# Kernel tuning notes

Hardware: AMD Instinct MI355X
Metric: run time of the kernel (lower is better)

## Reference

```python
import jax, jax.numpy as jnp
import numpy as np
from jax import lax

IMG = 224.0
IOU_THRESH = 0.5

def box_cxcywh_to_xyxy(b):
    cx, cy, w, h = b[..., 0], b[..., 1], b[..., 2], b[..., 3]
    return jnp.stack([cx - 0.5 * w, cy - 0.5 * h, cx + 0.5 * w, cy + 0.5 * h], axis=-1)

def box_iou(a, b):
    area_a = (a[:, 2] - a[:, 0]) * (a[:, 3] - a[:, 1])
    area_b = (b[:, 2] - b[:, 0]) * (b[:, 3] - b[:, 1])
    lt = jnp.maximum(a[:, None, :2], b[None, :, :2])
    rb = jnp.minimum(a[:, None, 2:], b[None, :, 2:])
    wh = jnp.clip(rb - lt, 0.0)
    inter = wh[..., 0] * wh[..., 1]
    return inter / (area_a[:, None] + area_b[None, :] - inter)

def gumbel_softmax(key, logits, axis, tau=1.0):
    # straight-through hard gumbel-softmax (matches torch hard=True)
    g = jax.random.gumbel(key, logits.shape, logits.dtype)
    y = jax.nn.softmax((logits + g) / tau, axis=axis)
    y_hard = jax.nn.one_hot(jnp.argmax(y, axis=axis), y.shape[axis], axis=axis, dtype=y.dtype)
    return y + lax.stop_gradient(y_hard - y)

def nms_indices(boxes, scores, thresh):
    # iterative greedy NMS, returns kept indices in descending-score order (as torchvision)
    n = boxes.shape[0]
    order = jnp.argsort(-scores)
    b = boxes[order]
    areas = (b[:, 2] - b[:, 0]) * (b[:, 3] - b[:, 1])
    pos = jnp.arange(n)
    def body(i, suppressed):
        bi = b[i]
        lt = jnp.maximum(bi[:2], b[:, :2])
        rb = jnp.minimum(bi[2:], b[:, 2:])
        wh = jnp.clip(rb - lt, 0.0)
        inter = wh[:, 0] * wh[:, 1]
        iou = inter / (areas[i] + areas - inter)
        sup = (iou > thresh) & (pos > i) & jnp.logical_not(suppressed[i])
        return suppressed | sup
    suppressed = lax.fori_loop(0, n, body, jnp.zeros((n,), bool))
    keep = np.asarray(jnp.logical_not(suppressed))
    return jnp.asarray(np.asarray(order)[keep])

def _keys():
    return jax.random.split(jax.random.key(42), 3)

def _boxes_and_scores(classencodings, pred_logits, pred_boxes, tgt_ids, batch_idx, tgt_bbox, k0):
    C = classencodings.shape[0]
    B, Q, D = pred_logits.shape
    similarity = jnp.einsum('bqd,cd->bqc', pred_logits, classencodings)
    out_scores = jnp.max(similarity, axis=-1)
    clt = gumbel_softmax(k0, similarity, axis=-1)                      # [B,Q,C] hard
    offx = jnp.arange(C, dtype=pred_logits.dtype) * IMG
    offy = jnp.arange(B, dtype=pred_logits.dtype) * IMG
    ox = jnp.sum(clt * offx, axis=-1)                                  # [B,Q]
    oy = jnp.broadcast_to(offy[:, None], (B, Q))
    out_off = jnp.tile(jnp.stack([ox, oy], axis=-1), (1, 1, 2))        # [B,Q,4]
    out_bbox = (box_cxcywh_to_xyxy(pred_boxes) + out_off).reshape(-1, 4)
    f = pred_logits.dtype
    gt_off = jnp.tile(jnp.stack([IMG * tgt_ids.astype(f), IMG * batch_idx.astype(f)], axis=-1), (1, 2))
    tb = box_cxcywh_to_xyxy(tgt_bbox) + gt_off                         # [N,4]
    return similarity, out_scores.reshape(-1), out_bbox, tb

def ce_diag(logits):
    # CrossEntropyLoss(mean) with targets arange(n)
    return -jnp.mean(jnp.diagonal(jax.nn.log_softmax(logits, axis=1)))

def _forward(classencodings, pred_logits, pred_boxes, pred_masks, tgt_masks, tgt_embs, tgt_bbox, tgt_ids, batch_idx, nms_idx):
    k0, k1, k2 = _keys()
    B, Q, D = pred_logits.shape
    N = tgt_embs.shape[0]
    W, H = tgt_masks.shape[-2:]
    similarity, out_scores, out_bbox, tb = _boxes_and_scores(classencodings, pred_logits, pred_boxes, tgt_ids, batch_idx, tgt_bbox, k0)
    kept = out_bbox[nms_idx]                                           # [K,4]
    K = kept.shape[0]
    iou = box_iou(kept, tb)
    iou = jnp.where(jnp.isnan(iou), 0.0, iou)
    gt_log = jax.nn.softmax(iou, axis=1)
    gt_one_hot = gumbel_softmax(k1, gt_log, axis=1)                    # [K,N]
    gt_sel = gt_one_hot.T @ kept                                       # [N,4]
    gt_ious = jnp.diagonal(box_iou(gt_sel, tb))
    out_embs = gt_one_hot.T @ pred_logits.reshape(-1, D)[nms_idx]      # [N,D]
    class_loss = ce_diag(tgt_embs @ out_embs.T) + ce_diag(out_embs @ tgt_embs.T)
    scores = jnp.einsum('bqd,nd->bqn', pred_logits, tgt_embs).reshape(B * Q, N)
    ind = gumbel_softmax(k2, scores, axis=0).T                         # [N,B*Q]
    om = (ind @ pred_masks.reshape(B * Q, -1)).reshape(N, W, H)
    overall_mask_loss = jnp.mean((om - tgt_masks) ** 2)
    ocm = jnp.einsum('qwh,bcq->bcwh', om, similarity) / om.shape[1]    # [B,Q,W,H] (N==C==Q)
    ocm = jax.nn.softmax(ocm, axis=1)
    batch_lookup = jax.nn.one_hot(batch_idx, B, dtype=pred_logits.dtype).T  # [B,N]
    gt_sim = tgt_embs @ classencodings.T                               # [N,C]
    tsim = batch_lookup[:, :, None] * gt_sim[None, :, :]               # [B,N,C]
    gt_cm = jnp.einsum('bnc,nwh->bcwh', tsim, tgt_masks)               # [B,C,W,H]
    inp = ocm.reshape(B, -1)
    tgt = gt_cm.reshape(B, -1)
    dice = jnp.mean(jnp.sum(inp * tgt) / (jnp.sum(inp, -1) + jnp.sum(tgt, -1) + 1e-6))
    l1 = jnp.abs(gt_sel - tb).sum()
    return jnp.stack([class_loss, dice, overall_mask_loss / K, (1.0 - gt_ious).sum() / K, l1 / K])

def setup_inputs():
    key = jax.random.key(0)
    ks = jax.random.split(key, 10)
    B, Q, C, N, D, W, H = 8, 300, 300, 300, 256, 96, 96
    return {
        'classencodings': jax.random.normal(ks[0], (C, D), jnp.float32),
        'pred_logits': jax.random.normal(ks[1], (B, Q, D), jnp.float32),
        'pred_boxes': jax.random.uniform(ks[2], (B, Q, 4), jnp.float32),
        'pred_masks': jax.random.normal(ks[3], (B * Q, W, H), jnp.float32),
        'tgt_masks': jax.random.uniform(ks[4], (N, W, H), jnp.float32),
        'tgt_embs': jax.random.normal(ks[5], (N, D), jnp.float32),
        'tgt_bbox': jax.random.uniform(ks[6], (N, 4), jnp.float32),
        'im_masks': jnp.ones((B, 224, 224), jnp.float32),
        'tgt_ids': jax.random.randint(ks[7], (N,), 0, C, jnp.int32),
        'batch_idx': jnp.sort(jax.random.randint(ks[8], (N,), 0, B, jnp.int32)),
    }

def reference(classencodings, pred_logits, pred_boxes, pred_masks, tgt_masks, tgt_embs, tgt_bbox, im_masks, tgt_ids, batch_idx):
    k0, _, _ = _keys()
    _, scores, out_bbox, _ = _boxes_and_scores(classencodings, pred_logits, pred_boxes, tgt_ids, batch_idx, tgt_bbox, k0)
    nms_idx = nms_indices(out_bbox, scores, IOU_THRESH)
    return _forward(classencodings, pred_logits, pred_boxes, pred_masks, tgt_masks, tgt_embs, tgt_bbox, tgt_ids, batch_idx, nms_idx)
```

## Files before the change

kernel.cpp:

```cpp
#include <hip/hip_runtime.h>
#include <stdint.h>

#define DEVFN __device__ __forceinline__

typedef unsigned short u16;
typedef short bf16x8 __attribute__((ext_vector_type(8)));
typedef float f32x4 __attribute__((ext_vector_type(4)));

constexpr int BB = 8, QQ = 300, CC = 300, NN = 300, DD = 256;
constexpr int WHX = 9216, BQ = 2400, SIMW = 600;
constexpr int QP = 320;
constexpr int CP = 304;
constexpr int KP = 96;
constexpr int NP = 416;
constexpr int CELLCAP = 300;

constexpr size_t F_SIMS   = 0;
constexpr size_t F_GTSIM  = F_SIMS   + (size_t)BQ*SIMW;
constexpr size_t F_MM     = F_GTSIM  + (size_t)NN*CC;
constexpr size_t F_SCORE  = F_MM     + (size_t)NN*NN;
constexpr size_t F_BBOX   = F_SCORE  + BQ;
constexpr size_t F_TB     = F_BBOX   + (size_t)BQ*4;
constexpr size_t F_SB     = F_TB     + (size_t)NN*4;
constexpr size_t F_SAREA  = F_SB     + (size_t)BQ*4;
constexpr size_t F_KB     = F_SAREA  + BQ;
constexpr size_t F_ROWSUM = F_KB     + (size_t)BQ*4;
constexpr size_t F_OE     = F_ROWSUM + NN;
constexpr size_t F_GSEL   = F_OE     + (size_t)NN*DD;
constexpr size_t F_MSUM   = F_GSEL   + (size_t)NN*4;
constexpr size_t F_STGT   = F_MSUM   + NN;
constexpr size_t F_SC     = F_STGT   + 8;
constexpr size_t F_CNT    = F_SC     + 16;
constexpr size_t F_ACCEND = F_CNT    + BQ;
constexpr size_t F_ORDER  = F_ACCEND;
constexpr size_t F_NMSIDX = F_ORDER  + BQ;
constexpr size_t F_SEL2   = F_NMSIDX + BQ;
constexpr size_t F_BSTART = F_SEL2   + NN;
constexpr size_t F_KINT   = F_BSTART + 16;
constexpr size_t F_CLS    = F_KINT   + 4;
constexpr size_t F_KEEPF  = F_CLS    + BQ;
constexpr size_t F_LIST   = F_KEEPF  + BQ;
constexpr size_t F_S2T    = F_LIST   + (size_t)BQ*CELLCAP;
constexpr size_t F_SIMTB  = ((F_S2T + (size_t)NN*BQ + 7) & ~(size_t)7);
constexpr size_t F_OMT    = F_SIMTB + (size_t)BB*CP*QP/2;
constexpr size_t F_TMT    = F_OMT   + (size_t)WHX*QP/2;
constexpr size_t F_GTP    = F_TMT   + (size_t)WHX*NP/2;
constexpr size_t F_TOTAL  = F_GTP   + (size_t)BB*CP*KP/2;

DEVFN uint32_t rotl32(uint32_t v, int r){ return (v << r) | (v >> (32 - r)); }

DEVFN void tf2x32(uint32_t k0, uint32_t k1, uint32_t x0, uint32_t x1,
                  uint32_t& o0, uint32_t& o1){
  uint32_t ks2 = k0 ^ k1 ^ 0x1BD11BDAu;
  x0 += k0; x1 += k1;
#define TFR(r) x0 += x1; x1 = rotl32(x1, r); x1 ^= x0;
  TFR(13) TFR(15) TFR(26) TFR(6)   x0 += k1;  x1 += ks2 + 1u;
  TFR(17) TFR(29) TFR(16) TFR(24)  x0 += ks2; x1 += k0  + 2u;
  TFR(13) TFR(15) TFR(26) TFR(6)   x0 += k0;  x1 += k1  + 3u;
  TFR(17) TFR(29) TFR(16) TFR(24)  x0 += k1;  x1 += ks2 + 4u;
  TFR(13) TFR(15) TFR(26) TFR(6)   x0 += ks2; x1 += k0  + 5u;
#undef TFR
  o0 = x0; o1 = x1;
}

DEVFN void subkey(int i, uint32_t& k0, uint32_t& k1){
  tf2x32(0u, 42u, 0u, (uint32_t)i, k0, k1);
}

DEVFN float gumbel32(uint32_t k0, uint32_t k1, uint32_t idx){
  uint32_t h, l; tf2x32(k0, k1, 0u, idx, h, l);
  uint32_t bits = h ^ l;
  float f = __uint_as_float((bits >> 9) | 0x3F800000u) - 1.0f;
  const float tiny = 1.17549435e-38f;
  float u = fmaxf(tiny, f + tiny);
  return -logf(-logf(u));
}

DEVFN float iou_xyxy(float ax1,float ay1,float ax2,float ay2,
                     float bx1,float by1,float bx2,float by2){
  float aa = (ax2-ax1)*(ay2-ay1);
  float ab = (bx2-bx1)*(by2-by1);
  float lx = fmaxf(ax1,bx1), ly = fmaxf(ay1,by1);
  float rx = fminf(ax2,bx2), ry = fminf(ay2,by2);
  float iw = fmaxf(rx-lx,0.f), ih = fmaxf(ry-ly,0.f);
  float in_ = iw*ih;
  return in_/(aa+ab-in_);
}

DEVFN u16 f2bf(float x){
  uint32_t u = __float_as_uint(x);
  uint32_t r = u + 0x7FFFu + ((u >> 16) & 1u);
  return (u16)(r >> 16);
}

DEVFN void gload_lds16(const u16* g, u16* l){
  __builtin_amdgcn_global_load_lds(
      (const __attribute__((address_space(1))) unsigned int*)g,
      (__attribute__((address_space(3))) unsigned int*)l,
      16, 0, 0);
}

__global__ __launch_bounds__(256) void k_gemm_t(
    const float* __restrict__ pl, const float* __restrict__ ce,
    const float* __restrict__ te, float* __restrict__ sims,
    float* __restrict__ gtsim, float* __restrict__ s2t){
  __shared__ float As[16][64];
  __shared__ float Bs[16][64];
  const int row0 = blockIdx.x * 64, col0 = blockIdx.y * 64;
  const int tid = threadIdx.x;
  const int lrow = tid >> 2, lk0 = (tid & 3) * 4;
  const int tr = tid >> 4, tc = tid & 15;

  float acc[4][4];
  #pragma unroll
  for (int i = 0; i < 4; i++)
    #pragma unroll
    for (int j = 0; j < 4; j++) acc[i][j] = 0.f;

  const float4 z4 = {0.f,0.f,0.f,0.f};
  const int grow = row0 + lrow;
  const int gcol = col0 + lrow;
  const float* arow = nullptr;
  if (grow < 2400) arow = pl + (size_t)grow * DD;
  else if (grow < 2700) arow = te + (size_t)(grow - 2400) * DD;
  const float* brow = nullptr;
  if (gcol < 300) brow = ce + (size_t)gcol * DD;
  else if (gcol < 600) brow = te + (size_t)(gcol - 300) * DD;

  float4 av = arow ? *(const float4*)(arow + lk0) : z4;
  float4 bv = brow ? *(const float4*)(brow + lk0) : z4;

  for (int step = 0; step < 16; step++){
    __syncthreads();
    #pragma unroll
    for (int j = 0; j < 4; j++){
      As[lk0 + j][lrow] = ((const float*)&av)[j];
      Bs[lk0 + j][lrow] = ((const float*)&bv)[j];
    }
    __syncthreads();
    if (step + 1 < 16){
      const int k0 = (step + 1) * 16;
      av = arow ? *(const float4*)(arow + k0 + lk0) : z4;
      bv = brow ? *(const float4*)(brow + k0 + lk0) : z4;
    }
    #pragma unroll
    for (int kk = 0; kk < 16; kk++){
      float4 a4 = *(const float4*)&As[kk][tr*4];
      float4 b4 = *(const float4*)&Bs[kk][tc*4];
      float a[4] = {a4.x,a4.y,a4.z,a4.w};
      float b[4] = {b4.x,b4.y,b4.z,b4.w};
      #pragma unroll
      for (int i = 0; i < 4; i++)
        #pragma unroll
        for (int j = 0; j < 4; j++)
          acc[i][j] = fmaf(a[i], b[j], acc[i][j]);
    }
  }

  #pragma unroll
  for (int i = 0; i < 4; i++){
    const int r = row0 + tr*4 + i;
    const int c0 = col0 + tc*4;
    if (r < 2400){
      if (c0 < 600){
        float4 o0 = {acc[i][0],acc[i][1],acc[i][2],acc[i][3]};
        *(float4*)(sims + (size_t)r*SIMW + c0) = o0;
        if (c0 >= 300){
          #pragma unroll
          for (int j = 0; j < 4; j++)
            s2t[(size_t)(c0 + j - 300)*BQ + r] = acc[i][j];
        }
      }
    } else if (r < 2700){
      const int n = r - 2400;
      #pragma unroll
      for (int j = 0; j < 4; j++){
        int c = c0 + j;
        if (c < 300) gtsim[(size_t)n*CC + c] = acc[i][j];
      }
    }
  }
}

__global__ __launch_bounds__(256) void k_post(
    const float* __restrict__ sims, const float* __restrict__ pb,
    const float* __restrict__ tbb, const int* __restrict__ tids,
    const int* __restrict__ bidx, const float* __restrict__ gtsim,
    float* __restrict__ score, float* __restrict__ bbox,
    float* __restrict__ tb, float* __restrict__ rowsum,
    int* __restrict__ clsout){
  int bq = blockIdx.x, tid = threadIdx.x;
  __shared__ float sv[256];
  __shared__ int   si[256];
  const int i2 = tid + 256;
  float v1 = (tid < CC) ? sims[(size_t)bq*SIMW + tid] : -INFINITY;
  float v2 = (i2  < CC) ? sims[(size_t)bq*SIMW + i2]  : -INFINITY;
  sv[tid] = fmaxf(v1, v2); __syncthreads();
  for (int s = 128; s > 0; s >>= 1){ if (tid < s) sv[tid] = fmaxf(sv[tid], sv[tid+s]); __syncthreads(); }
  if (tid == 0) score[bq] = sv[0];
  __syncthreads();
  uint32_t gk0, gk1; subkey(0, gk0, gk1);
  float y1 = (tid < CC) ? v1 + gumbel32(gk0, gk1, (uint32_t)(bq*CC + tid)) : -INFINITY;
  float y2 = (i2  < CC) ? v2 + gumbel32(gk0, gk1, (uint32_t)(bq*CC + i2))  : -INFINITY;
  float ym; int yi;
  if (y2 > y1){ ym = y2; yi = i2; } else { ym = y1; yi = tid; }
  sv[tid] = ym; si[tid] = yi; __syncthreads();
  for (int s = 128; s > 0; s >>= 1){
    if (tid < s){
      float ov = sv[tid+s]; int oi = si[tid+s];
      if (ov > sv[tid] || (ov == sv[tid] && oi < si[tid])){ sv[tid] = ov; si[tid] = oi; }
    }
    __syncthreads();
  }
  if (tid == 0){
    int cls = si[0];
    clsout[bq] = cls;
    float ox = 224.0f * (float)cls;
    float oy = 224.0f * (float)(bq / QQ);
    float cx = pb[bq*4+0], cy = pb[bq*4+1], ww = pb[bq*4+2], hh = pb[bq*4+3];
    bbox[bq*4+0] = cx - 0.5f*ww + ox;
    bbox[bq*4+1] = cy - 0.5f*hh + oy;
    bbox[bq*4+2] = cx + 0.5f*ww + ox;
    bbox[bq*4+3] = cy + 0.5f*hh + oy;
  }
  if (bq < NN){
    __syncthreads();
    float r1 = (tid < CC) ? gtsim[(size_t)bq*CC + tid] : 0.f;
    float r2 = (i2  < CC) ? gtsim[(size_t)bq*CC + i2]  : 0.f;
    sv[tid] = r1 + r2; __syncthreads();
    for (int s = 128; s > 0; s >>= 1){ if (tid < s) sv[tid] += sv[tid+s]; __syncthreads(); }
    if (tid == 0) rowsum[bq] = sv[0];
    if (tid == 1){
      float gx = 224.0f * (float)tids[bq], gy = 224.0f * (float)bidx[bq];
      float cx = tbb[bq*4+0], cy = tbb[bq*4+1], ww = tbb[bq*4+2], hh = tbb[bq*4+3];
      tb[bq*4+0] = cx - 0.5f*ww + gx;
      tb[bq*4+1] = cy - 0.5f*hh + gy;
      tb[bq*4+2] = cx + 0.5f*ww + gx;
      tb[bq*4+3] = cy + 0.5f*hh + gy;
    }
  }
}

__global__ __launch_bounds__(256) void k_rankgather(
    const float* __restrict__ score, const float* __restrict__ bbox,
    const int* __restrict__ cls, const int* __restrict__ bidx,
    int* __restrict__ order, float* __restrict__ sb,
    int* __restrict__ bstart, int* __restrict__ cnt,
    int* __restrict__ list){
  const int t = blockIdx.x;
  const int tid = threadIdx.x;
  const float st = score[t];
  int c = 0;
  for (int j = tid; j < BQ; j += 256){
    float sj = score[j];
    c += (sj > st) || (sj == st && j < t);
  }
  __shared__ int red[256];
  red[tid] = c; __syncthreads();
  for (int s = 128; s > 0; s >>= 1){
    if (tid < s) red[tid] += red[tid+s];
    __syncthreads();
  }
  if (tid == 0){
    int r = red[0];
    order[r] = t;
    float x1 = bbox[t*4+0], y1 = bbox[t*4+1], x2 = bbox[t*4+2], y2 = bbox[t*4+3];
    sb[r*4+0] = x1; sb[r*4+1] = y1; sb[r*4+2] = x2; sb[r*4+3] = y2;
    int key = (t / QQ) * CC + cls[t];
    int slot = atomicAdd(&cnt[key], 1);
    list[(size_t)key*CELLCAP + slot] = r;
  }
  if (t == 0 && tid >= 32 && tid < 41){
    int b = tid - 32, cb = 0;
    for (int n = 0; n < NN; n++) cb += (bidx[n] < b);
    bstart[b] = cb;
  }
}

__global__ __launch_bounds__(256) void k_cellnms(
    const float* __restrict__ sb, const int* __restrict__ cnt,
    const int* __restrict__ list, int* __restrict__ keepf){
  int key = blockIdx.x*256 + threadIdx.x;
  if (key >= BB*CC) return;
  int m = cnt[key];
  if (m <= 0) return;
  const int* lst = list + (size_t)key*CELLCAP;
  unsigned long long keptmask = 0ull;
  int prevp = -1;
  for (int a = 0; a < m; a++){
    int pa = 0x7fffffff;
    for (int j = 0; j < m; j++){
      int pj = lst[j];
      if (pj > prevp && pj < pa) pa = pj;
    }
    prevp = pa;
    float4 A = ((const float4*)sb)[pa];
    float areaA = (A.z-A.x)*(A.w-A.y);
    bool kept = true;
    int pbprev = -1;
    for (int b2 = 0; b2 < a; b2++){
      int pb = 0x7fffffff;
      for (int j = 0; j < m; j++){
        int pj = lst[j];
        if (pj > pbprev && pj < pb) pb = pj;
      }
      pbprev = pb;
      bool keptb = (m <= 64) ? (((keptmask >> b2) & 1ull) != 0ull) : (keepf[pb] != 0);
      if (!keptb) continue;
      float4 B = ((const float4*)sb)[pb];
      float areaB = (B.z-B.x)*(B.w-B.y);
      float lx = fmaxf(A.x,B.x), ly = fmaxf(A.y,B.y);
      float rx = fminf(A.z,B.z), ry = fminf(A.w,B.w);
      float iw = fmaxf(rx-lx,0.f), ih = fmaxf(ry-ly,0.f);
      float inter = iw*ih;
      if (inter/(areaA + areaB - inter) > 0.5f){ kept = false; break; }
    }
    if (m <= 64 && kept) keptmask |= (1ull << a);
    keepf[pa] = kept ? 1 : 0;
  }
}

__global__ __launch_bounds__(256) void k_compact(
    const int* __restrict__ keepflag, const int* __restrict__ order,
    const float* __restrict__ sb, int* __restrict__ nmsidx,
    float* __restrict__ kb, int* __restrict__ kint){
  __shared__ int csum[256];
  int tid = threadIdx.x;
  int p0 = tid*10;
  int keepf[10];
  int cnt = 0;
  #pragma unroll
  for (int d = 0; d < 10; d++){
    int p = p0 + d;
    int k = 0;
    if (p < BQ) k = keepflag[p];
    keepf[d] = k; cnt += k;
  }
  csum[tid] = cnt; __syncthreads();
  for (int s = 1; s < 256; s <<= 1){
    int add = (tid >= s) ? csum[tid - s] : 0;
    __syncthreads();
    csum[tid] += add;
    __syncthreads();
  }
  int pos = csum[tid] - cnt;
  #pragma unroll
  for (int d = 0; d < 10; d++){
    if (keepf[d]){
      int p = p0 + d;
      nmsidx[pos] = order[p];
      ((float4*)kb)[pos] = ((const float4*)sb)[p];
      pos++;
    }
  }
  if (tid == 255) kint[0] = csum[255];
}

__global__ __launch_bounds__(512) void k_gtsel(
    const float* __restrict__ kb, const float* __restrict__ tb,
    const int* __restrict__ nmsidx, const float* __restrict__ pl,
    const int* __restrict__ kint, float* __restrict__ gsel,
    float* __restrict__ oe){
  int k = blockIdx.x;
  if (k >= kint[0]) return;
  int tid = threadIdx.x;
  __shared__ float sv[512];
  __shared__ int   si[512];
  float4 a = ((const float4*)kb)[k];
  float iou = -INFINITY;
  if (tid < NN){
    float4 t = ((const float4*)tb)[tid];
    iou = iou_xyxy(a.x,a.y,a.z,a.w, t.x,t.y,t.z,t.w);
    if (iou != iou) iou = 0.f;
  }
  sv[tid] = iou; __syncthreads();
  for (int s = 256; s > 0; s >>= 1){ if (tid < s) sv[tid] = fmaxf(sv[tid], sv[tid+s]); __syncthreads(); }
  float m = sv[0]; __syncthreads();
  float e = (tid < NN) ? expf(iou - m) : 0.f;
  sv[tid] = e; __syncthreads();
  for (int s = 256; s > 0; s >>= 1){ if (tid < s) sv[tid] += sv[tid+s]; __syncthreads(); }
  float S = sv[0]; __syncthreads();
  uint32_t gk0, gk1; subkey(1, gk0, gk1);
  float y = (tid < NN) ? (e / S + gumbel32(gk0, gk1, (uint32_t)(k*NN + tid))) : -INFINITY;
  sv[tid] = y; si[tid] = tid; __syncthreads();
  for (int s = 256; s > 0; s >>= 1){
    if (tid < s){
      float ov = sv[tid+s]; int oi = si[tid+s];
      if (ov > sv[tid] || (ov == sv[tid] && oi < si[tid])){ sv[tid] = ov; si[tid] = oi; }
    }
    __syncthreads();
  }
  int sel = si[0];
  if (tid < 4) atomicAdd(&gsel[sel*4 + tid], ((const float*)&a)[tid]);
  if (tid < DD) atomicAdd(&oe[(size_t)sel*DD + tid], pl[(size_t)nmsidx[k]*DD + tid]);
}

__global__ __launch_bounds__(256) void k_m_t(
    const float* __restrict__ te, const float* __restrict__ oe,
    float* __restrict__ M){
  __shared__ float As[16][32];
  __shared__ float Bs[16][32];
  const int row0 = blockIdx.x * 32, col0 = blockIdx.y * 32;
  const int tid = threadIdx.x;
  const int lr = tid >> 3, lk0 = (tid & 7) * 2;
  const int tr = tid >> 4, tc = tid & 15;
  float acc[2][2] = {{0.f,0.f},{0.f,0.f}};
  const float* arow = (row0 + lr < NN) ? te + (size_t)(row0 + lr)*DD : nullptr;
  const float* brow = (col0 + lr < NN) ? oe + (size_t)(col0 + lr)*DD : nullptr;
  for (int step = 0; step < 16; step++){
    const int k0 = step*16;
    float2 a2 = arow ? *(const float2*)(arow + k0 + lk0) : float2{0.f,0.f};
    float2 b2 = brow ? *(const float2*)(brow + k0 + lk0) : float2{0.f,0.f};
    __syncthreads();
    As[lk0][lr] = a2.x; As[lk0+1][lr] = a2.y;
    Bs[lk0][lr] = b2.x; Bs[lk0+1][lr] = b2.y;
    __syncthreads();
    #pragma unroll
    for (int kk = 0; kk < 16; kk++){
      float a0 = As[kk][tr*2], a1 = As[kk][tr*2+1];
      float b0 = Bs[kk][tc*2], b1 = Bs[kk][tc*2+1];
      acc[0][0] = fmaf(a0,b0,acc[0][0]);
      acc[0][1] = fmaf(a0,b1,acc[0][1]);
      acc[1][0] = fmaf(a1,b0,acc[1][0]);
      acc[1][1] = fmaf(a1,b1,acc[1][1]);
    }
  }
  #pragma unroll
  for (int i = 0; i < 2; i++){
    int r = row0 + tr*2 + i;
    if (r >= NN) continue;
    #pragma unroll
    for (int j = 0; j < 2; j++){
      int c = col0 + tc*2 + j;
      if (c < NN) M[(size_t)r*NN + c] = acc[i][j];
    }
  }
}

__global__ __launch_bounds__(64) void k_ce(
    const float* __restrict__ M, float* __restrict__ sc){
  int i = blockIdx.x, lane = threadIdx.x;
  float m = -INFINITY;
  for (int j = lane; j < NN; j += 64) m = fmaxf(m, M[(size_t)i*NN + j]);
  for (int o = 32; o > 0; o >>= 1) m = fmaxf(m, __shfl_xor(m, o));
  float s = 0.f;
  for (int j = lane; j < NN; j += 64) s += expf(M[(size_t)i*NN + j] - m);
  for (int o = 32; o > 0; o >>= 1) s += __shfl_xor(s, o);
  float lr = m + logf(s);
  float m2 = -INFINITY;
  for (int j = lane; j < NN; j += 64) m2 = fmaxf(m2, M[(size_t)j*NN + i]);
  for (int o = 32; o > 0; o >>= 1) m2 = fmaxf(m2, __shfl_xor(m2, o));
  float s2 = 0.f;
  for (int j = lane; j < NN; j += 64) s2 += expf(M[(size_t)j*NN + i] - m2);
  for (int o = 32; o > 0; o >>= 1) s2 += __shfl_xor(s2, o);
  float lc = m2 + logf(s2);
  if (lane == 0){
    float d = M[(size_t)i*NN + i];
    atomicAdd(&sc[0], lr - d);
    atomicAdd(&sc[1], lc - d);
  }
}

__global__ __launch_bounds__(256) void k_sel2(
    const float* __restrict__ s2t, int* __restrict__ sel2){
  int n = blockIdx.x, tid = threadIdx.x;
  uint32_t gk0, gk1; subkey(2, gk0, gk1);
  float best = -INFINITY; int bi = 0x7fffffff;
  for (int r = tid; r < BQ; r += 256){
    float v = s2t[(size_t)n*BQ + r] + gumbel32(gk0, gk1, (uint32_t)(r*NN + n));
    if (v > best){ best = v; bi = r; }
  }
  __shared__ float sv[256];
  __shared__ int   si[256];
  sv[tid] = best; si[tid] = bi; __syncthreads();
  for (int s = 128; s > 0; s >>= 1){
    if (tid < s){
      float ov = sv[tid+s]; int oi = si[tid+s];
      if (ov > sv[tid] || (ov == sv[tid] && oi < si[tid])){ sv[tid] = ov; si[tid] = oi; }
    }
    __syncthreads();
  }
  if (tid == 0) sel2[n] = si[0];
}

constexpr int PB_SIMT = 400;
constexpr int PB_OMT  = 1440;
constexpr int PB_TMT  = 1872;
constexpr int PB_GTP  = 114;
constexpr int PB_OM   = 2700;
__global__ __launch_bounds__(256) void k_pack(
    const float* __restrict__ sims, const float* __restrict__ pm,
    const float* __restrict__ tm, const float* __restrict__ gtsim,
    const int* __restrict__ sel2, const int* __restrict__ bstart,
    u16* __restrict__ simTb, u16* __restrict__ omT,
    u16* __restrict__ tmT, u16* __restrict__ gtp,
    float* __restrict__ msum, float* __restrict__ sc){
  __shared__ float ld[32][65];
  const int blk = blockIdx.x;
  const int tid = threadIdx.x;

  if (blk < PB_SIMT){
    int bx = blk % 10, by = (blk / 10) % 5, b = blk / 50;
    int q0 = bx*32, c0 = by*64;
    for (int i = tid; i < 32*64; i += 256){
      int qi = i >> 6, ci = i & 63;
      int q = q0 + qi, c = c0 + ci;
      ld[qi][ci] = (q < QQ && c < CC) ? sims[((size_t)b*QQ + q)*SIMW + c] : 0.f;
    }
    __syncthreads();
    int cloc = tid >> 2, j0 = (tid & 3)*8;
    int c = c0 + cloc;
    if (c < CP){
      u16 tmp[8];
      #pragma unroll
      for (int j = 0; j < 8; j++) tmp[j] = f2bf(ld[j0+j][cloc]);
      *(uint4*)(simTb + ((size_t)b*CP + c)*QP + q0 + j0) = *(const uint4*)tmp;
    }
  } else if (blk < PB_SIMT + PB_OMT){
    int r = blk - PB_SIMT;
    int q0 = (r % 10)*32, wh0 = (r / 10)*64;
    for (int i = tid; i < 32*64; i += 256){
      int qi = i >> 6, wi = i & 63;
      int q = q0 + qi;
      ld[qi][wi] = (q < QQ) ? pm[(size_t)sel2[q]*WHX + wh0 + wi] * (1.0f/96.0f) : 0.f;
    }
    __syncthreads();
    int wloc = tid >> 2, j0 = (tid & 3)*8;
    u16 tmp[8];
    #pragma unroll
    for (int j = 0; j < 8; j++) tmp[j] = f2bf(ld[j0+j][wloc]);
    *(uint4*)(omT + (size_t)(wh0+wloc)*QP + q0 + j0) = *(const uint4*)tmp;
  } else if (blk < PB_SIMT + PB_OMT + PB_TMT){
    int r = blk - PB_SIMT - PB_OMT;
    int n0 = (r % 13)*32, wh0 = (r / 13)*64;
    for (int i = tid; i < 32*64; i += 256){
      int ni = i >> 6, wi = i & 63;
      int n = n0 + ni;
      ld[ni][wi] = (n < NN) ? tm[(size_t)n*WHX + wh0 + wi] : 0.f;
    }
    __syncthreads();
    int wloc = tid >> 2, j0 = (tid & 3)*8;
    u16 tmp[8];
    #pragma unroll
    for (int j = 0; j < 8; j++) tmp[j] = f2bf(ld[j0+j][wloc]);
    *(uint4*)(tmT + (size_t)(wh0+wloc)*NP + n0 + j0) = *(const uint4*)tmp;
  } else if (blk < PB_SIMT + PB_OMT + PB_TMT + PB_GTP){
    int g = (blk - PB_SIMT - PB_OMT - PB_TMT)*256 + tid;
    int b = g / (CP*(KP/8));
    int rem = g - b*(CP*(KP/8));
    int c = rem / (KP/8);
    int kg = rem % (KP/8);
    int n0 = bstart[b], n1 = bstart[b+1];
    int kst = n0 & ~7;
    u16 tmp[8];
    #pragma unroll
    for (int j = 0; j < 8; j++){
      int n = kst + kg*8 + j;
      float v = (n >= n0 && n < n1 && c < CC) ? gtsim[(size_t)n*CC + c] : 0.f;
      tmp[j] = f2bf(v);
    }
    *(uint4*)(gtp + ((size_t)b*CP + c)*KP + kg*8) = *(const uint4*)tmp;
  } else {
    int nb = blk - (PB_SIMT + PB_OMT + PB_TMT + PB_GTP);
    int n = nb / 9, ch = nb % 9;
    int c0 = ch*1024 + tid*4;
    const float4 o4 = *(const float4*)(pm + (size_t)sel2[n]*WHX + c0);
    const float4 t4 = *(const float4*)(tm + (size_t)n*WHX + c0);
    float dx = o4.x-t4.x, dy = o4.y-t4.y, dz = o4.z-t4.z, dw = o4.w-t4.w;
    float d2 = dx*dx + dy*dy + dz*dz + dw*dw;
    float ts = t4.x + t4.y + t4.z + t4.w;
    float* r1 = &ld[0][0];
    float* r2 = r1 + 256;
    r1[tid] = d2; r2[tid] = ts; __syncthreads();
    for (int s = 128; s > 0; s >>= 1){
      if (tid < s){ r1[tid] += r1[tid+s]; r2[tid] += r2[tid+s]; }
      __syncthreads();
    }
    if (tid == 0){ atomicAdd(&sc[2], r1[0]); atomicAdd(&msum[n], r2[0]); }
  }
}

constexpr int ALDS = 32;
__global__ __launch_bounds__(256) void k_zsoft(
    const u16* __restrict__ simTb, const u16* __restrict__ omT,
    const u16* __restrict__ gtp, const u16* __restrict__ tmT,
    const int* __restrict__ bstart, float* __restrict__ sc){
  const int bid = blockIdx.x;
  const int xcd = bid & 7;
  const int r9  = bid >> 3;
  const int tile = xcd * 18 + (r9 % 18);
  const int b    = r9 / 18;
  const int tid = threadIdx.x;
  const int w = tid >> 6, l = tid & 63;
  const int lrow = l & 15, lgrp = l >> 4;
  const int col = tile*64 + w*16 + lrow;

  __shared__ u16 As[2][CP*ALDS];
  __shared__ float red[256];

  const u16* Ab = simTb + (size_t)b*CP*QP;
  int srcoff[5];
  #pragma unroll
  for (int i = 0; i < 5; i++){
    int p = (w*5 + i)*64 + l;
    int row = p >> 2, cs = p & 3;
    int g = cs ^ ((row >> 1) & 3);
    srcoff[i] = row*QP + g*8;
  }
  const int nIss = (w == 3) ? 4 : 5;
  const int roff = (lgrp ^ ((lrow >> 1) & 3)) << 3;
  const u16* pB = omT + (size_t)col*QP + lgrp*8;

  #pragma unroll
  for (int i = 0; i < 5; i++){
    if (i < nIss) gload_lds16(Ab + srcoff[i], &As[0][(w*5+i)*512]);
  }
  bf16x8 bcur = *(const bf16x8*)(pB);

  f32x4 acc[19];
  #pragma unroll
  for (int t = 0; t < 19; t++) acc[t] = (f32x4){0.f,0.f,0.f,0.f};
  __syncthreads();

  for (int ks = 0; ks < 10; ks++){
    const int cur = ks & 1;
    bf16x8 bnext;
    if (ks + 1 < 10){
      const int ko = (ks + 1) * 32;
      #pragma unroll
      for (int i = 0; i < 5; i++){
        if (i < nIss) gload_lds16(Ab + srcoff[i] + ko, &As[cur ^ 1][(w*5+i)*512]);
      }
      bnext = *(const bf16x8*)(pB + ko);
    }
    __builtin_amdgcn_s_setprio(1);
    #pragma unroll
    for (int t = 0; t < 19; t++){
      bf16x8 af = *(const bf16x8*)&As[cur][t*16*ALDS + lrow*ALDS + roff];
      acc[t] = __builtin_amdgcn_mfma_f32_16x16x32_bf16(af, bcur, acc[t], 0, 0, 0);
    }
    __builtin_amdgcn_s_setprio(0);
    bcur = bnext;
    __syncthreads();
  }

  const int n0 = bstart[b];
  const int kst = n0 & ~7;
  const u16* tB = tmT + (size_t)col*NP + kst + lgrp*8;
  bf16x8 b2a = *(const bf16x8*)(tB);
  bf16x8 b2b = *(const bf16x8*)(tB + 32);
  bf16x8 b2c = *(const bf16x8*)(tB + 64);
  const u16* A2 = gtp + (size_t)b*CP*KP + (size_t)lrow*KP + lgrp*8;
  bf16x8 ca0 = *(const bf16x8*)(A2);
  bf16x8 ca1 = *(const bf16x8*)(A2 + 32);
  bf16x8 ca2 = *(const bf16x8*)(A2 + 64);
  bf16x8 da0 = *(const bf16x8*)(A2 + 16*KP);
  bf16x8 da1 = *(const bf16x8*)(A2 + 16*KP + 32);
  bf16x8 da2 = *(const bf16x8*)(A2 + 16*KP + 64);

  float lmax = -INFINITY;
  #pragma unroll
  for (int t = 0; t < 19; t++){
    if (t == 18 && lgrp == 3) continue;
    lmax = fmaxf(lmax, fmaxf(fmaxf(acc[t][0], acc[t][1]), fmaxf(acc[t][2], acc[t][3])));
  }
  lmax = fmaxf(lmax, __shfl_xor(lmax, 16));
  lmax = fmaxf(lmax, __shfl_xor(lmax, 32));
  float ls = 0.f;
  #pragma unroll
  for (int t = 0; t < 19; t++){
    if (t == 18 && lgrp == 3){
      acc[t] = (f32x4){0.f,0.f,0.f,0.f};
      continue;
    }
    float p0 = __expf(acc[t][0] - lmax);
    float p1 = __expf(acc[t][1] - lmax);
    float p2 = __expf(acc[t][2] - lmax);
    float p3 = __expf(acc[t][3] - lmax);
    acc[t][0] = p0; acc[t][1] = p1; acc[t][2] = p2; acc[t][3] = p3;
    ls += p0 + p1 + p2 + p3;
  }
  float S = ls;
  S += __shfl_xor(S, 16);
  S += __shfl_xor(S, 32);
  float inv = 1.f / S;

  float dl = 0.f;
  #pragma unroll
  for (int t = 0; t < 19; t++){
    f32x4 rr = (f32x4){0.f,0.f,0.f,0.f};
    rr = __builtin_amdgcn_mfma_f32_16x16x32_bf16(ca0, b2a, rr, 0, 0, 0);
    rr = __builtin_amdgcn_mfma_f32_16x16x32_bf16(ca1, b2b, rr, 0, 0, 0);
    rr = __builtin_amdgcn_mfma_f32_16x16x32_bf16(ca2, b2c, rr, 0, 0, 0);
    dl += acc[t][0]*rr[0] + acc[t][1]*rr[1] + acc[t][2]*rr[2] + acc[t][3]*rr[3];
    ca0 = da0; ca1 = da1; ca2 = da2;
    if (t + 2 < 19){
      const u16* ar = A2 + (size_t)(t + 2)*16*KP;
      da0 = *(const bf16x8*)(ar);
      da1 = *(const bf16x8*)(ar + 32);
      da2 = *(const bf16x8*)(ar + 64);
    }
  }
  dl *= inv;

  red[tid] = dl; __syncthreads();
  for (int s = 128; s > 0; s >>= 1){
    if (tid < s) red[tid] += red[tid+s];
    __syncthreads();
  }
  if (tid == 0) atomicAdd(&sc[5], red[0]);
}

__global__ __launch_bounds__(512) void k_final3(
    const float* __restrict__ gsel, const float* __restrict__ tb,
    const int* __restrict__ bidx, const float* __restrict__ rowsum,
    const float* __restrict__ msum, const float* __restrict__ sc,
    const int* __restrict__ kint, float* __restrict__ out){
  int tid = threadIdx.x;
  __shared__ float s1[512], s2[512];
  __shared__ float stgt[8];
  if (tid < 8) stgt[tid] = 0.f;
  __syncthreads();
  float a1 = 0.f, a2 = 0.f;
  if (tid < NN){
    float4 g = ((const float4*)gsel)[tid];
    float4 t = ((const float4*)tb)[tid];
    float iou = iou_xyxy(g.x,g.y,g.z,g.w, t.x,t.y,t.z,t.w);
    a1 = 1.f - iou;
    a2 = fabsf(g.x-t.x) + fabsf(g.y-t.y) + fabsf(g.z-t.z) + fabsf(g.w-t.w);
    atomicAdd(&stgt[bidx[tid]], rowsum[tid] * msum[tid]);
  }
  s1[tid] = a1; s2[tid] = a2; __syncthreads();
  for (int s = 256; s > 0; s >>= 1){
    if (tid < s){ s1[tid] += s1[tid+s]; s2[tid] += s2[tid+s]; }
    __syncthreads();
  }
  if (tid == 0){
    float K = (float)kint[0];
    float cls = sc[0]/300.f + sc[1]/300.f;
    float stot = sc[5];
    float dice = 0.f;
    for (int b = 0; b < 8; b++) dice += stot / (9216.0f + stgt[b] + 1e-6f);
    dice *= (1.0f/8.0f);
    out[0] = cls;
    out[1] = dice;
    out[2] = (sc[2] / 2764800.0f) / K;
    out[3] = s1[0] / K;
    out[4] = s2[0] / K;
  }
}

extern "C" void kernel_launch(void* const* d_in, const int* in_sizes, int n_in,
                              void* d_out, int out_size, void* d_ws, size_t ws_size,
                              hipStream_t stream) {
  const float* ce  = (const float*)d_in[0];
  const float* pl  = (const float*)d_in[1];
  const float* pb  = (const float*)d_in[2];
  const float* pm  = (const float*)d_in[3];
  const float* tm  = (const float*)d_in[4];
  const float* te  = (const float*)d_in[5];
  const float* tbb = (const float*)d_in[6];
  const int*  tids = (const int*)d_in[8];
  const int*  bidx = (const int*)d_in[9];
  float* out = (float*)d_out;
  float* w = (float*)d_ws;

  if (ws_size < F_TOTAL * sizeof(float)) return;

  float* SIMS   = w + F_SIMS;
  float* GTSIM  = w + F_GTSIM;
  float* MM     = w + F_MM;
  float* SCORE  = w + F_SCORE;
  float* BBOX   = w + F_BBOX;
  float* TBOX   = w + F_TB;
  float* SB     = w + F_SB;
  float* KB     = w + F_KB;
  float* ROWSUM = w + F_ROWSUM;
  float* OE     = w + F_OE;
  float* GSEL   = w + F_GSEL;
  float* MSUM   = w + F_MSUM;
  float* SC     = w + F_SC;
  float* S2T    = w + F_S2T;
  int*   CNT    = (int*)(w + F_CNT);
  int*   ORDER  = (int*)(w + F_ORDER);
  int*   NMSIDX = (int*)(w + F_NMSIDX);
  int*   SEL2   = (int*)(w + F_SEL2);
  int*   BSTART = (int*)(w + F_BSTART);
  int*   KINT   = (int*)(w + F_KINT);
  int*   CLS    = (int*)(w + F_CLS);
  int*   KEEPF  = (int*)(w + F_KEEPF);
  int*   LIST   = (int*)(w + F_LIST);
  u16* SIMTB = (u16*)(w + F_SIMTB);
  u16* OMT   = (u16*)(w + F_OMT);
  u16* TMT   = (u16*)(w + F_TMT);
  u16* GTP   = (u16*)(w + F_GTP);

  hipMemsetAsync(w + F_OE, 0, (F_ACCEND - F_OE) * sizeof(float), stream);

  k_gemm_t<<<dim3(43, 10), 256, 0, stream>>>(pl, ce, te, SIMS, GTSIM, S2T);
  k_post<<<BQ, 256, 0, stream>>>(SIMS, pb, tbb, tids, bidx, GTSIM, SCORE, BBOX, TBOX, ROWSUM, CLS);
  k_rankgather<<<BQ, 256, 0, stream>>>(SCORE, BBOX, CLS, bidx, ORDER, SB, BSTART, CNT, LIST);
  k_sel2<<<NN, 256, 0, stream>>>(S2T, SEL2);
  k_pack<<<PB_SIMT + PB_OMT + PB_TMT + PB_GTP + PB_OM, 256, 0, stream>>>(
      SIMS, pm, tm, GTSIM, SEL2, BSTART, SIMTB, OMT, TMT, GTP, MSUM, SC);
  k_cellnms<<<(BB*CC + 255)/256, 256, 0, stream>>>(SB, CNT, LIST, KEEPF);
  k_compact<<<1, 256, 0, stream>>>(KEEPF, ORDER, SB, NMSIDX, KB, KINT);
  k_gtsel<<<BQ, 512, 0, stream>>>(KB, TBOX, NMSIDX, pl, KINT, GSEL, OE);
  k_m_t<<<dim3(10, 10), 256, 0, stream>>>(te, OE, MM);
  k_ce<<<NN, 64, 0, stream>>>(MM, SC);
  k_zsoft<<<dim3((WHX/64) * BB), 256, 0, stream>>>(SIMTB, OMT, GTP, TMT, BSTART, SC);
  k_final3<<<1, 512, 0, stream>>>(GSEL, TBOX, bidx, ROWSUM, MSUM, SC, KINT, out);
}
```

Before: 268.0 us.

## Split zsoft warp tiles into 2x2 row/column halves with cross-warp softmax reduction

Re-tiles the k_zsoft MFMA work so each warp computes two 16-column groups over half of the C rows, instead of one column group over all 19 row tiles. Each A fragment read from LDS now feeds two MFMAs, which halves LDS A traffic per MFMA. The softmax max and sum are combined across warp pairs through shared memory. CP is padded to 320 so the rows split evenly into 10+10 tiles. This adds extra barriers and a padded row tile that has to be masked, and the second-stage MFMA work per column group is now split across warps.

Result: no change. 273.2 us (+1.9%).

```diff
diff --git a/kernel.cpp b/kernel.cpp
--- a/kernel.cpp
+++ b/kernel.cpp
@@ -10,7 +10,7 @@
 constexpr int BB = 8, QQ = 300, CC = 300, NN = 300, DD = 256;
 constexpr int WHX = 9216, BQ = 2400, SIMW = 600;
 constexpr int QP = 320;
-constexpr int CP = 304;
+constexpr int CP = 320;
 constexpr int KP = 96;
 constexpr int NP = 416;
 constexpr int CELLCAP = 300;
@@ -486,7 +486,7 @@
 constexpr int PB_SIMT = 400;
 constexpr int PB_OMT  = 1440;
 constexpr int PB_TMT  = 1872;
-constexpr int PB_GTP  = 114;
+constexpr int PB_GTP  = 120;
 constexpr int PB_OM   = 2700;
 __global__ __launch_bounds__(256) void k_pack(
     const float* __restrict__ sims, const float* __restrict__ pm,
@@ -593,7 +593,9 @@
   const int tid = threadIdx.x;
   const int w = tid >> 6, l = tid & 63;
   const int lrow = l & 15, lgrp = l >> 4;
-  const int col = tile*64 + w*16 + lrow;
+  const int cg = w >> 1, rh = w & 1;
+  const int col0 = tile*64 + cg*32 + lrow;
+  const int t0 = rh * 10;
 
   __shared__ u16 As[2][CP*ALDS];
   __shared__ float red[256];
@@ -607,101 +609,127 @@
     int g = cs ^ ((row >> 1) & 3);
     srcoff[i] = row*QP + g*8;
   }
-  const int nIss = (w == 3) ? 4 : 5;
   const int roff = (lgrp ^ ((lrow >> 1) & 3)) << 3;
-  const u16* pB = omT + (size_t)col*QP + lgrp*8;
-
-  #pragma unroll
-  for (int i = 0; i < 5; i++){
-    if (i < nIss) gload_lds16(Ab + srcoff[i], &As[0][(w*5+i)*512]);
-  }
-  bf16x8 bcur = *(const bf16x8*)(pB);
-
-  f32x4 acc[19];
-  #pragma unroll
-  for (int t = 0; t < 19; t++) acc[t] = (f32x4){0.f,0.f,0.f,0.f};
+  const u16* pB0 = omT + (size_t)col0*QP + lgrp*8;
+  const u16* pB1 = omT + (size_t)(col0+16)*QP + lgrp*8;
+
+  #pragma unroll
+  for (int i = 0; i < 5; i++) gload_lds16(Ab + srcoff[i], &As[0][(w*5+i)*512]);
+  bf16x8 bcur0 = *(const bf16x8*)pB0;
+  bf16x8 bcur1 = *(const bf16x8*)pB1;
+
+  f32x4 acc0[10], acc1[10];
+  #pragma unroll
+  for (int t = 0; t < 10; t++){
+    acc0[t] = (f32x4){0.f,0.f,0.f,0.f};
+    acc1[t] = (f32x4){0.f,0.f,0.f,0.f};
+  }
   __syncthreads();
 
   for (int ks = 0; ks < 10; ks++){
     const int cur = ks & 1;
-    bf16x8 bnext;
+    bf16x8 bnext0, bnext1;
     if (ks + 1 < 10){
       const int ko = (ks + 1) * 32;
       #pragma unroll
-      for (int i = 0; i < 5; i++){
-        if (i < nIss) gload_lds16(Ab + srcoff[i] + ko, &As[cur ^ 1][(w*5+i)*512]);
-      }
-      bnext = *(const bf16x8*)(pB + ko);
+      for (int i = 0; i < 5; i++) gload_lds16(Ab + srcoff[i] + ko, &As[cur ^ 1][(w*5+i)*512]);
+      bnext0 = *(const bf16x8*)(pB0 + ko);
+      bnext1 = *(const bf16x8*)(pB1 + ko);
     }
     __builtin_amdgcn_s_setprio(1);
     #pragma unroll
-    for (int t = 0; t < 19; t++){
-      bf16x8 af = *(const bf16x8*)&As[cur][t*16*ALDS + lrow*ALDS + roff];
-      acc[t] = __builtin_amdgcn_mfma_f32_16x16x32_bf16(af, bcur, acc[t], 0, 0, 0);
+    for (int t = 0; t < 10; t++){
+      bf16x8 af = *(const bf16x8*)&As[cur][(t0 + t)*16*ALDS + lrow*ALDS + roff];
+      acc0[t] = __builtin_amdgcn_mfma_f32_16x16x32_bf16(af, bcur0, acc0[t], 0, 0, 0);
+      acc1[t] = __builtin_amdgcn_mfma_f32_16x16x32_bf16(af, bcur1, acc1[t], 0, 0, 0);
     }
     __builtin_amdgcn_s_setprio(0);
-    bcur = bnext;
-    __syncthreads();
-  }
+    bcur0 = bnext0; bcur1 = bnext1;
+    __syncthreads();
+  }
+
+  float lmax0 = -INFINITY, lmax1 = -INFINITY;
+  #pragma unroll
+  for (int t = 0; t < 10; t++){
+    int g = t0 + t;
+    if (g == 19 || (g == 18 && lgrp == 3)) continue;
+    lmax0 = fmaxf(lmax0, fmaxf(fmaxf(acc0[t][0], acc0[t][1]), fmaxf(acc0[t][2], acc0[t][3])));
+    lmax1 = fmaxf(lmax1, fmaxf(fmaxf(acc1[t][0], acc1[t][1]), fmaxf(acc1[t][2], acc1[t][3])));
+  }
+  lmax0 = fmaxf(lmax0, __shfl_xor(lmax0, 16));
+  lmax0 = fmaxf(lmax0, __shfl_xor(lmax0, 32));
+  lmax1 = fmaxf(lmax1, __shfl_xor(lmax1, 16));
+  lmax1 = fmaxf(lmax1, __shfl_xor(lmax1, 32));
+  if (l < 16){ red[w*32 + l] = lmax0; red[w*32 + 16 + l] = lmax1; }
+  __syncthreads();
+  float m0 = fmaxf(lmax0, red[(w^1)*32 + lrow]);
+  float m1 = fmaxf(lmax1, red[(w^1)*32 + 16 + lrow]);
+  __syncthreads();
+
+  float ls0 = 0.f, ls1 = 0.f;
+  #pragma unroll
+  for (int t = 0; t < 10; t++){
+    int g = t0 + t;
+    if (g == 19 || (g == 18 && lgrp == 3)){
+      acc0[t] = (f32x4){0.f,0.f,0.f,0.f};
+      acc1[t] = (f32x4){0.f,0.f,0.f,0.f};
+      continue;
+    }
+    #pragma unroll
+    for (int q = 0; q < 4; q++){
+      float p0 = __expf(acc0[t][q] - m0);
+      float p1 = __expf(acc1[t][q] - m1);
+      acc0[t][q] = p0; acc1[t][q] = p1;
+      ls0 += p0; ls1 += p1;
+    }
+  }
+  ls0 += __shfl_xor(ls0, 16); ls0 += __shfl_xor(ls0, 32);
+  ls1 += __shfl_xor(ls1, 16); ls1 += __shfl_xor(ls1, 32);
+  if (l < 16){ red[w*32 + l] = ls0; red[w*32 + 16 + l] = ls1; }
+  __syncthreads();
+  float S0 = ls0 + red[(w^1)*32 + lrow];
+  float S1 = ls1 + red[(w^1)*32 + 16 + lrow];
+  __syncthreads();
+  float inv0 = 1.f / S0, inv1 = 1.f / S1;
 
   const int n0 = bstart[b];
   const int kst = n0 & ~7;
-  const u16* tB = tmT + (size_t)col*NP + kst + lgrp*8;
-  bf16x8 b2a = *(const bf16x8*)(tB);
-  bf16x8 b2b = *(const bf16x8*)(tB + 32);
-  bf16x8 b2c = *(const bf16x8*)(tB + 64);
   const u16* A2 = gtp + (size_t)b*CP*KP + (size_t)lrow*KP + lgrp*8;
-  bf16x8 ca0 = *(const bf16x8*)(A2);
-  bf16x8 ca1 = *(const bf16x8*)(A2 + 32);
-  bf16x8 ca2 = *(const bf16x8*)(A2 + 64);
-  bf16x8 da0 = *(const bf16x8*)(A2 + 16*KP);
-  bf16x8 da1 = *(const bf16x8*)(A2 + 16*KP + 32);
-  bf16x8 da2 = *(const bf16x8*)(A2 + 16*KP + 64);
-
-  float lmax = -INFINITY;
-  #pragma unroll
-  for (int t = 0; t < 19; t++){
-    if (t == 18 && lgrp == 3) continue;
-    lmax = fmaxf(lmax, fmaxf(fmaxf(acc[t][0], acc[t][1]), fmaxf(acc[t][2], acc[t][3])));
-  }
-  lmax = fmaxf(lmax, __shfl_xor(lmax, 16));
-  lmax = fmaxf(lmax, __shfl_xor(lmax, 32));
-  float ls = 0.f;
-  #pragma unroll
-  for (int t = 0; t < 19; t++){
-    if (t == 18 && lgrp == 3){
-      acc[t] = (f32x4){0.f,0.f,0.f,0.f};
-      continue;
-    }
-    float p0 = __expf(acc[t][0] - lmax);
-    float p1 = __expf(acc[t][1] - lmax);
-    float p2 = __expf(acc[t][2] - lmax);
-    float p3 = __expf(acc[t][3] - lmax);
-    acc[t][0] = p0; acc[t][1] = p1; acc[t][2] = p2; acc[t][3] = p3;
-    ls += p0 + p1 + p2 + p3;
-  }
-  float S = ls;
-  S += __shfl_xor(S, 16);
-  S += __shfl_xor(S, 32);
-  float inv = 1.f / S;
-
   float dl = 0.f;
-  #pragma unroll
-  for (int t = 0; t < 19; t++){
-    f32x4 rr = (f32x4){0.f,0.f,0.f,0.f};
-    rr = __builtin_amdgcn_mfma_f32_16x16x32_bf16(ca0, b2a, rr, 0, 0, 0);
-    rr = __builtin_amdgcn_mfma_f32_16x16x32_bf16(ca1, b2b, rr, 0, 0, 0);
-    rr = __builtin_amdgcn_mfma_f32_16x16x32_bf16(ca2, b2c, rr, 0, 0, 0);
-    dl += acc[t][0]*rr[0] + acc[t][1]*rr[1] + acc[t][2]*rr[2] + acc[t][3]*rr[3];
-    ca0 = da0; ca1 = da1; ca2 = da2;
-    if (t + 2 < 19){
-      const u16* ar = A2 + (size_t)(t + 2)*16*KP;
-      da0 = *(const bf16x8*)(ar);
-      da1 = *(const bf16x8*)(ar + 32);
-      da2 = *(const bf16x8*)(ar + 64);
-    }
-  }
-  dl *= inv;
+  {
+    const u16* tB = tmT + (size_t)col0*NP + kst + lgrp*8;
+    bf16x8 b2a = *(const bf16x8*)(tB);
+    bf16x8 b2b = *(const bf16x8*)(tB + 32);
+    bf16x8 b2c = *(const bf16x8*)(tB + 64);
+    float d = 0.f;
+    #pragma unroll
+    for (int t = 0; t < 10; t++){
+      const u16* ar = A2 + (size_t)(t0 + t)*16*KP;
+      f32x4 rr = (f32x4){0.f,0.f,0.f,0.f};
+      rr = __builtin_amdgcn_mfma_f32_16x16x32_bf16(*(const bf16x8*)(ar),      b2a, rr, 0, 0, 0);
+      rr = __builtin_amdgcn_mfma_f32_16x16x32_bf16(*(const bf16x8*)(ar + 32), b2b, rr, 0, 0, 0);
+      rr = __builtin_amdgcn_mfma_f32_16x16x32_bf16(*(const bf16x8*)(ar + 64), b2c, rr, 0, 0, 0);
+      d += acc0[t][0]*rr[0] + acc0[t][1]*rr[1] + acc0[t][2]*rr[2] + acc0[t][3]*rr[3];
+    }
+    dl += d * inv0;
+  }
+  {
+    const u16* tB = tmT + (size_t)(col0+16)*NP + kst + lgrp*8;
+    bf16x8 b2a = *(const bf16x8*)(tB);
+    bf16x8 b2b = *(const bf16x8*)(tB + 32);
+    bf16x8 b2c = *(const bf16x8*)(tB + 64);
+    float d = 0.f;
+    #pragma unroll
+    for (int t = 0; t < 10; t++){
+      const u16* ar = A2 + (size_t)(t0 + t)*16*KP;
+      f32x4 rr = (f32x4){0.f,0.f,0.f,0.f};
+      rr = __builtin_amdgcn_mfma_f32_16x16x32_bf16(*(const bf16x8*)(ar),      b2a, rr, 0, 0, 0);
+      rr = __builtin_amdgcn_mfma_f32_16x16x32_bf16(*(const bf16x8*)(ar + 32), b2b, rr, 0, 0, 0);
+      rr = __builtin_amdgcn_mfma_f32_16x16x32_bf16(*(const bf16x8*)(ar + 64), b2c, rr, 0, 0, 0);
+      d += acc1[t][0]*rr[0] + acc1[t][1]*rr[1] + acc1[t][2]*rr[2] + acc1[t][3]*rr[3];
+    }
+    dl += d * inv1;
+  }
 
   red[tid] = dl; __syncthreads();
   for (int s = 128; s > 0; s >>= 1){
```
